# Performance work log

Hardware: AMD Instinct MI355X
Metric: run time of the kernel (lower is better)

The kernel has to match this reference:

```python
import jax, jax.numpy as jnp
import numpy as np

T, B, D, H = 512, 64, 1024, 1024

def setup_inputs() -> dict:
    key = jax.random.key(0)
    k1, k2, k3, k4, k5 = jax.random.split(key, 5)
    scale_x = np.sqrt(6.0) / np.sqrt(D + 4 * H)
    scale_h = np.sqrt(6.0) / np.sqrt(H + 4 * H)
    x_data = jax.random.normal(k1, (T, B, D), dtype=jnp.float32)
    # binary mask (1 = valid token), as used for variable-length sequences
    x_mask = (jax.random.uniform(k2, (T, B)) < 0.9).astype(jnp.float32)
    Wx = jax.random.uniform(k3, (4 * H, D), minval=-scale_x, maxval=scale_x, dtype=jnp.float32)
    bx = jax.random.uniform(k4, (4 * H,), minval=-scale_x, maxval=scale_x, dtype=jnp.float32)
    Wh = jax.random.uniform(k5, (4 * H, H), minval=-scale_h, maxval=scale_h, dtype=jnp.float32)
    return {"x_data": x_data, "x_mask": x_mask, "Wx": Wx, "bx": bx, "Wh": Wh}

def _lstm_forward(x_data, x_mask, Wx, bx, Wh):
    # Precompute input projections for all timesteps in one GEMM: [T,B,4H]
    xg = jnp.einsum('tbd,gd->tbg', x_data, Wx) + bx
    Hh = Wh.shape[1]

    def step(carry, inp):
        htm, ctm = carry
        xg_t, m_t = inp  # [B,4H], [B]
        gates = xg_t + htm @ Wh.T
        ig, fg, og, ct = jnp.split(gates, 4, axis=1)
        ig = jax.nn.sigmoid(ig)
        fg = jax.nn.sigmoid(fg)
        og = jax.nn.sigmoid(og)
        ct = jnp.tanh(ct)
        ct = fg * ctm + ig * ct
        ht = og * jnp.tanh(ct)
        m = m_t[:, None]
        ct = ct * m + ctm * (1.0 - m)
        ht = ht * m + htm * (1.0 - m)
        return (ht, ct), ht

    h0 = jnp.zeros((x_data.shape[1], Hh), dtype=x_data.dtype)
    c0 = jnp.zeros((x_data.shape[1], Hh), dtype=x_data.dtype)
    _, output = jax.lax.scan(step, (h0, c0), (xg, x_mask))
    return output  # [T,B,H]

def reference(x_data, x_mask, Wx, bx, Wh):
    return _lstm_forward(x_data, x_mask, Wx, bx, Wh)
```

## Files before the change

kernel.cpp:

```cpp
#include <hip/hip_runtime.h>
#include <hip/hip_bf16.h>

using f32x4  = __attribute__((ext_vector_type(4))) float;
using bf16x8 = __attribute__((ext_vector_type(8))) __bf16;
using u64    = unsigned long long;

#define T_DIM 512
#define B_DIM 64
#define D_DIM 1024
#define H_DIM 1024
#define G_DIM 4096
#define NWG   128
#define WGT   512

__global__ void f32_to_bf16_kernel(const float* __restrict__ src,
                                   __bf16* __restrict__ dst, long n) {
    long i = ((long)blockIdx.x * blockDim.x + threadIdx.x) * 8;
    if (i + 8 <= n) {
        f32x4 a = *(const f32x4*)(src + i);
        f32x4 b = *(const f32x4*)(src + i + 4);
        bf16x8 o;
        o[0] = (__bf16)a[0]; o[1] = (__bf16)a[1];
        o[2] = (__bf16)a[2]; o[3] = (__bf16)a[3];
        o[4] = (__bf16)b[0]; o[5] = (__bf16)b[1];
        o[6] = (__bf16)b[2]; o[7] = (__bf16)b[3];
        *(bf16x8*)(dst + i) = o;
    }
}

#define BM 128
#define BN 128
#define BK 64

__global__ __launch_bounds__(256) void gemm_xg_kernel(
    const __bf16* __restrict__ A,
    const __bf16* __restrict__ W,
    const float* __restrict__ bias,
    float* __restrict__ C,
    int M)
{
    (void)M;
    __shared__ __bf16 sA[BM * BK];
    __shared__ __bf16 sB[BN * BK];

    const int tid = threadIdx.x;
    const int wv  = tid >> 6;
    const int l   = tid & 63;
    const int wy  = wv >> 1, wx = wv & 1;
    const int bm  = blockIdx.y * BM;
    const int bn  = blockIdx.x * BN;
    const int n   = l & 15;
    const int q   = l >> 4;

    const int srow  = l >> 3;
    const int skoff = (l & 7) * 8;

    f32x4 acc[4][4];
    #pragma unroll
    for (int mt = 0; mt < 4; ++mt)
        #pragma unroll
        for (int nt = 0; nt < 4; ++nt)
            acc[mt][nt] = (f32x4){0.f, 0.f, 0.f, 0.f};

    for (int kt = 0; kt < D_DIM / BK; ++kt) {
        const int k0 = kt * BK;
        #pragma unroll
        for (int j = 0; j < 4; ++j) {
            const int rbase = (j * 4 + wv) * 8;
            const __bf16* ga = A + (long)(bm + rbase + srow) * D_DIM + k0 + skoff;
            const __bf16* gb = W + (long)(bn + rbase + srow) * D_DIM + k0 + skoff;
            __builtin_amdgcn_global_load_lds(
                (const __attribute__((address_space(1))) void*)ga,
                (__attribute__((address_space(3))) void*)(sA + rbase * BK), 16, 0, 0);
            __builtin_amdgcn_global_load_lds(
                (const __attribute__((address_space(1))) void*)gb,
                (__attribute__((address_space(3))) void*)(sB + rbase * BK), 16, 0, 0);
        }
        __syncthreads();

        #pragma unroll
        for (int ks = 0; ks < 2; ++ks) {
            bf16x8 af[4], bfr[4];
            #pragma unroll
            for (int mt = 0; mt < 4; ++mt) {
                int row = wy * 64 + mt * 16 + n;
                af[mt] = *(const bf16x8*)(sA + row * BK + ks * 32 + q * 8);
            }
            #pragma unroll
            for (int nt = 0; nt < 4; ++nt) {
                int col = wx * 64 + nt * 16 + n;
                bfr[nt] = *(const bf16x8*)(sB + col * BK + ks * 32 + q * 8);
            }
            #pragma unroll
            for (int mt = 0; mt < 4; ++mt)
                #pragma unroll
                for (int nt = 0; nt < 4; ++nt)
                    acc[mt][nt] = __builtin_amdgcn_mfma_f32_16x16x32_bf16(
                        af[mt], bfr[nt], acc[mt][nt], 0, 0, 0);
        }
        __syncthreads();
    }

    #pragma unroll
    for (int nt = 0; nt < 4; ++nt) {
        int col = bn + wx * 64 + nt * 16 + n;
        float b = bias[col];
        #pragma unroll
        for (int mt = 0; mt < 4; ++mt) {
            #pragma unroll
            for (int r = 0; r < 4; ++r) {
                int row = bm + wy * 64 + mt * 16 + q * 4 + r;
                C[(long)row * G_DIM + col] = acc[mt][nt][r] + b;
            }
        }
    }
}

__device__ __forceinline__ float fast_tanh(float x) {
    return 1.0f - 2.0f / (__expf(2.0f * x) + 1.0f);
}

__device__ __forceinline__ void grid_barrier(unsigned* __restrict__ flags,
                                             unsigned target, int tid, int wgid) {
    __syncthreads();
    if (tid == 0)
        __hip_atomic_store(&flags[wgid * 16], target, __ATOMIC_RELAXED,
                           __HIP_MEMORY_SCOPE_AGENT);
    if (tid < 64) {
        for (;;) {
            unsigned v0 = __hip_atomic_load(&flags[tid * 16],
                                            __ATOMIC_RELAXED, __HIP_MEMORY_SCOPE_AGENT);
            unsigned v1 = __hip_atomic_load(&flags[(tid + 64) * 16],
                                            __ATOMIC_RELAXED, __HIP_MEMORY_SCOPE_AGENT);
            if (__all((v0 >= target) & (v1 >= target))) break;
            __builtin_amdgcn_s_sleep(1);
        }
    }
    __syncthreads();
    __atomic_signal_fence(__ATOMIC_ACQUIRE);
}

__global__ __launch_bounds__(WGT)
__attribute__((amdgpu_waves_per_eu(2, 2)))
void lstm_scan_kernel(
    const __bf16* __restrict__ Whb,
    const float* __restrict__ xg,
    const float* __restrict__ mask,
    float* __restrict__ cst,
    __bf16* __restrict__ hbuf,
    float* __restrict__ out,
    unsigned* __restrict__ flags,
    int t0, int tc)
{
    __shared__ __align__(16) char shh[32768];
    __shared__ float sg[16][132];
    __shared__ unsigned short hp[16][32];

    const int tid  = threadIdx.x;
    const int wgid = blockIdx.x;
    const int rblk = wgid >> 5;
    const int ublk = wgid & 31;
    const int wv   = tid >> 6;
    const int l    = tid & 63;
    const int n    = l & 15;
    const int q    = l >> 4;
    const int gw   = wv >> 1;
    const int ch   = wv & 1;

    const int colg = gw * H_DIM + ublk * 32 + ch * 16 + n;

    bf16x8 breg[32];
    #pragma unroll
    for (int kk = 0; kk < 32; ++kk)
        breg[kk] = *(const bf16x8*)(Whb + (long)colg * H_DIM + kk * 32 + q * 8);

    const int grow_l = tid >> 5;
    const int u      = tid & 31;
    const int grow   = rblk * 16 + grow_l;
    const int ucol   = ublk * 32 + u;

    float c_r, h_r;
    if (t0 == 0) { c_r = 0.0f; h_r = 0.0f; }
    else {
        c_r = cst[grow * H_DIM + ucol];
        h_r = out[((long)(t0 - 1) * B_DIM + grow) * H_DIM + ucol];
    }

    float xc0, xc1, xc2, xc3, mkc;
    {
        const float* xr = xg + (long)grow * G_DIM + ucol;
        xc0 = xr[0]; xc1 = xr[H_DIM]; xc2 = xr[2 * H_DIM]; xc3 = xr[3 * H_DIM];
        mkc = mask[t0 * B_DIM + grow];
    }

    const int srow_lo = (l >> 3);
    const int sv      = l & 7;
    const int sq      = (l >> 1) & 3;
    const int sb      = (l & 1) * 8;

    for (int t = 0; t < tc; ++t) {
        const int gt = t0 + t;
        const __bf16* hread = hbuf + (long)(gt & 1) * (B_DIM * H_DIM);
        __bf16* hwrite = hbuf + (long)((gt + 1) & 1) * (B_DIM * H_DIM);
        const u64* h64 = (const u64*)hread;

        u64 hold[8];
        #pragma unroll
        for (int j = 0; j < 4; ++j) {
            const int kk = wv * 4 + j;
            hold[j * 2]     = __hip_atomic_load(
                h64 + (long)(rblk * 16 + srow_lo) * 256 + kk * 8 + sv,
                __ATOMIC_RELAXED, __HIP_MEMORY_SCOPE_AGENT);
            hold[j * 2 + 1] = __hip_atomic_load(
                h64 + (long)(rblk * 16 + 8 + srow_lo) * 256 + kk * 8 + sv,
                __ATOMIC_RELAXED, __HIP_MEMORY_SCOPE_AGENT);
        }
        #pragma unroll
        for (int j = 0; j < 4; ++j) {
            const int kk = wv * 4 + j;
            *(u64*)(shh + kk * 1024 + sq * 256 + srow_lo * 16 + sb)       = hold[j * 2];
            *(u64*)(shh + kk * 1024 + sq * 256 + (8 + srow_lo) * 16 + sb) = hold[j * 2 + 1];
        }
        __syncthreads();

        f32x4 ac0 = {0.f,0.f,0.f,0.f}, ac1 = {0.f,0.f,0.f,0.f};
        #pragma unroll
        for (int kk = 0; kk < 32; kk += 2) {
            bf16x8 f0 = *(const bf16x8*)(shh + (kk + 0) * 1024 + q * 256 + n * 16);
            bf16x8 f1 = *(const bf16x8*)(shh + (kk + 1) * 1024 + q * 256 + n * 16);
            ac0 = __builtin_amdgcn_mfma_f32_16x16x32_bf16(f0, breg[kk + 0], ac0, 0, 0, 0);
            ac1 = __builtin_amdgcn_mfma_f32_16x16x32_bf16(f1, breg[kk + 1], ac1, 0, 0, 0);
        }
        f32x4 acc = ac0 + ac1;

        {
            const int cw = gw * 32 + ch * 16 + n;
            #pragma unroll
            for (int r = 0; r < 4; ++r)
                sg[q * 4 + r][cw] = acc[r];
        }
        __syncthreads();

        float ig = xc0 + sg[grow_l][u];
        float fg = xc1 + sg[grow_l][32 + u];
        float og = xc2 + sg[grow_l][64 + u];
        float gg = xc3 + sg[grow_l][96 + u];

        float i_s = 1.0f / (1.0f + __expf(-ig));
        float f_s = 1.0f / (1.0f + __expf(-fg));
        float o_s = 1.0f / (1.0f + __expf(-og));
        float g_t = fast_tanh(gg);
        float c_new = f_s * c_r + i_s * g_t;
        float h_new = o_s * fast_tanh(c_new);
        float c_f = mkc * c_new + (1.0f - mkc) * c_r;
        float h_f = mkc * h_new + (1.0f - mkc) * h_r;
        c_r = c_f;
        h_r = h_f;

        hp[grow_l][u] = __builtin_bit_cast(unsigned short, (__bf16)h_f);
        __syncthreads();
        if (tid < 128) {
            const int prow = tid >> 3, pseg = tid & 7;
            u64 pk = *(const u64*)(&hp[prow][pseg * 4]);
            u64* dp = (u64*)((unsigned short*)hwrite +
                             (long)(rblk * 16 + prow) * H_DIM + ublk * 32 + pseg * 4);
            __hip_atomic_store(dp, pk, __ATOMIC_RELAXED, __HIP_MEMORY_SCOPE_AGENT);
        }

        out[((long)gt * B_DIM + grow) * H_DIM + ucol] = h_f;
        if (t == tc - 1) cst[grow * H_DIM + ucol] = c_f;

        if (t + 1 < tc) {
            const float* xr = xg + ((long)(t + 1) * B_DIM + grow) * G_DIM + ucol;
            xc0 = xr[0]; xc1 = xr[H_DIM]; xc2 = xr[2 * H_DIM]; xc3 = xr[3 * H_DIM];
            mkc = mask[(gt + 1) * B_DIM + grow];
        }

        grid_barrier(flags, (unsigned)(gt + 1), tid, wgid);
    }
}

extern "C" void kernel_launch(void* const* d_in, const int* in_sizes, int n_in,
                              void* d_out, int out_size, void* d_ws, size_t ws_size,
                              hipStream_t stream)
{
    (void)in_sizes; (void)n_in; (void)out_size;
    const float* x     = (const float*)d_in[0];
    const float* xmask = (const float*)d_in[1];
    const float* Wx    = (const float*)d_in[2];
    const float* bx    = (const float*)d_in[3];
    const float* Wh    = (const float*)d_in[4];
    float* out = (float*)d_out;

    char* ws = (char*)d_ws;
    __bf16*   Whb   = (__bf16*)(ws);
    __bf16*   Wxb   = (__bf16*)(ws + 8388608);
    __bf16*   hb    = (__bf16*)(ws + 16777216);
    float*    cst   = (float*)(ws + 16777216 + 262144);
    unsigned* flags = (unsigned*)(ws + 16777216 + 524288);
    char* dyn = ws + 16777216 + 1048576;

    long avail = (long)ws_size - (16777216L + 1048576L);
    const long per_t = (long)B_DIM * D_DIM * 2 + (long)B_DIM * G_DIM * 4;
    long Tc = avail > 0 ? avail / per_t : 2;
    if (Tc > T_DIM) Tc = T_DIM;
    Tc &= ~1L;
    if (Tc < 2) Tc = 2;

    __bf16* xb = (__bf16*)dyn;
    float*  xg = (float*)(dyn + Tc * (long)B_DIM * D_DIM * 2);

    hipMemsetAsync(ws + 16777216, 0, 1048576, stream);

    {
        long nw = (long)G_DIM * D_DIM;
        int nb = (int)(nw / 8 / 256);
        f32_to_bf16_kernel<<<nb, 256, 0, stream>>>(Wx, Wxb, nw);
        f32_to_bf16_kernel<<<nb, 256, 0, stream>>>(Wh, Whb, nw);
    }

    for (int t0 = 0; t0 < T_DIM; t0 += (int)Tc) {
        int tc = (int)((T_DIM - t0 < Tc) ? (long)(T_DIM - t0) : Tc);

        long nx = (long)tc * B_DIM * D_DIM;
        f32_to_bf16_kernel<<<(int)(nx / 8 / 256), 256, 0, stream>>>(
            x + (long)t0 * B_DIM * D_DIM, xb, nx);

        dim3 gg(G_DIM / BN, (tc * B_DIM) / BM);
        gemm_xg_kernel<<<gg, 256, 0, stream>>>(xb, Wxb, bx, xg, tc * B_DIM);

        const __bf16* Whb_a = Whb;
        const float*  xg_a  = xg;
        const float*  mask_a = xmask;
        float*  cst_a = cst;
        __bf16* hb_a  = hb;
        float*  out_a = out;
        unsigned* fl_a = flags;
        int t0_a = t0, tc_a = tc;
        void* args[] = {(void*)&Whb_a, (void*)&xg_a, (void*)&mask_a,
                        (void*)&cst_a, (void*)&hb_a, (void*)&out_a,
                        (void*)&fl_a, (void*)&t0_a, (void*)&tc_a};
        hipLaunchCooperativeKernel((void*)lstm_scan_kernel, dim3(NWG), dim3(WGT),
                                   args, 0, stream);
    }
}
```

Measured before the change: 2.532 ms.

## Remap gate columns per wave and narrow grid barrier to row-block peers

Each wave now computes all four gates for its own 4 hidden units, so the gate combine stays in a per-wave shared buffer. This removes two workgroup-wide __syncthreads per step, and h is packed with lane shuffles instead of a shared staging buffer. The grid barrier now waits only on the 32 workgroups that share the same batch row block, since only they produce the h rows this block reads. In exchange the out stores become vectorized but come from a quarter of the lanes, and correctness depends on the row-block independence of the recurrence.

```diff
diff --git a/kernel.cpp b/kernel.cpp
--- a/kernel.cpp
+++ b/kernel.cpp
@@ -121,18 +121,18 @@
 }
 
 __device__ __forceinline__ void grid_barrier(unsigned* __restrict__ flags,
-                                             unsigned target, int tid, int wgid) {
+                                             unsigned target, int tid,
+                                             int wgid, int rblk) {
     __syncthreads();
     if (tid == 0)
         __hip_atomic_store(&flags[wgid * 16], target, __ATOMIC_RELAXED,
                            __HIP_MEMORY_SCOPE_AGENT);
     if (tid < 64) {
+        const unsigned* fp = &flags[(rblk * 32 + (tid & 31)) * 16];
         for (;;) {
-            unsigned v0 = __hip_atomic_load(&flags[tid * 16],
-                                            __ATOMIC_RELAXED, __HIP_MEMORY_SCOPE_AGENT);
-            unsigned v1 = __hip_atomic_load(&flags[(tid + 64) * 16],
-                                            __ATOMIC_RELAXED, __HIP_MEMORY_SCOPE_AGENT);
-            if (__all((v0 >= target) & (v1 >= target))) break;
+            unsigned v = __hip_atomic_load(fp, __ATOMIC_RELAXED,
+                                           __HIP_MEMORY_SCOPE_AGENT);
+            if (__all(v >= target)) break;
             __builtin_amdgcn_s_sleep(1);
         }
     }
@@ -153,8 +153,7 @@
     int t0, int tc)
 {
     __shared__ __align__(16) char shh[32768];
-    __shared__ float sg[16][132];
-    __shared__ unsigned short hp[16][32];
+    __shared__ float sg[8][16 * 17];
 
     const int tid  = threadIdx.x;
     const int wgid = blockIdx.x;
@@ -164,20 +163,18 @@
     const int l    = tid & 63;
     const int n    = l & 15;
     const int q    = l >> 4;
-    const int gw   = wv >> 1;
-    const int ch   = wv & 1;
-
-    const int colg = gw * H_DIM + ublk * 32 + ch * 16 + n;
+
+    const int colg = ((n >> 2) << 10) + ublk * 32 + wv * 4 + (n & 3);
 
     bf16x8 breg[32];
     #pragma unroll
     for (int kk = 0; kk < 32; ++kk)
         breg[kk] = *(const bf16x8*)(Whb + (long)colg * H_DIM + kk * 32 + q * 8);
 
-    const int grow_l = tid >> 5;
-    const int u      = tid & 31;
-    const int grow   = rblk * 16 + grow_l;
-    const int ucol   = ublk * 32 + u;
+    const int rloc = l >> 2;
+    const int ui   = l & 3;
+    const int grow = rblk * 16 + rloc;
+    const int ucol = ublk * 32 + wv * 4 + ui;
 
     float c_r, h_r;
     if (t0 == 0) { c_r = 0.0f; h_r = 0.0f; }
@@ -199,6 +196,10 @@
     const int sb      = (l & 1) * 8;
 
     for (int t = 0; t < tc; ++t) {
+        #pragma unroll
+        for (int kk = 0; kk < 32; ++kk)
+            asm volatile("" : "+v"(breg[kk]));
+
         const int gt = t0 + t;
         const __bf16* hread = hbuf + (long)(gt & 1) * (B_DIM * H_DIM);
         __bf16* hwrite = hbuf + (long)((gt + 1) & 1) * (B_DIM * H_DIM);
@@ -233,18 +234,14 @@
         }
         f32x4 acc = ac0 + ac1;
 
-        {
-            const int cw = gw * 32 + ch * 16 + n;
-            #pragma unroll
-            for (int r = 0; r < 4; ++r)
-                sg[q * 4 + r][cw] = acc[r];
-        }
-        __syncthreads();
-
-        float ig = xc0 + sg[grow_l][u];
-        float fg = xc1 + sg[grow_l][32 + u];
-        float og = xc2 + sg[grow_l][64 + u];
-        float gg = xc3 + sg[grow_l][96 + u];
+        #pragma unroll
+        for (int r = 0; r < 4; ++r)
+            sg[wv][(q * 4 + r) * 17 + n] = acc[r];
+
+        float ig = xc0 + sg[wv][rloc * 17 + 0  + ui];
+        float fg = xc1 + sg[wv][rloc * 17 + 4  + ui];
+        float og = xc2 + sg[wv][rloc * 17 + 8  + ui];
+        float gg = xc3 + sg[wv][rloc * 17 + 12 + ui];
 
         float i_s = 1.0f / (1.0f + __expf(-ig));
         float f_s = 1.0f / (1.0f + __expf(-fg));
@@ -257,17 +254,24 @@
         c_r = c_f;
         h_r = h_f;
 
-        hp[grow_l][u] = __builtin_bit_cast(unsigned short, (__bf16)h_f);
-        __syncthreads();
-        if (tid < 128) {
-            const int prow = tid >> 3, pseg = tid & 7;
-            u64 pk = *(const u64*)(&hp[prow][pseg * 4]);
+        const int base = l & ~3;
+        float v0 = __shfl(h_f, base + 0);
+        float v1 = __shfl(h_f, base + 1);
+        float v2 = __shfl(h_f, base + 2);
+        float v3 = __shfl(h_f, base + 3);
+        if (ui == 0) {
+            f32x4 ov = {v0, v1, v2, v3};
+            *(f32x4*)(out + ((long)gt * B_DIM + grow) * H_DIM + ublk * 32 + wv * 4) = ov;
+            unsigned short b0 = __builtin_bit_cast(unsigned short, (__bf16)v0);
+            unsigned short b1 = __builtin_bit_cast(unsigned short, (__bf16)v1);
+            unsigned short b2 = __builtin_bit_cast(unsigned short, (__bf16)v2);
+            unsigned short b3 = __builtin_bit_cast(unsigned short, (__bf16)v3);
+            u64 pk = (u64)b0 | ((u64)b1 << 16) | ((u64)b2 << 32) | ((u64)b3 << 48);
             u64* dp = (u64*)((unsigned short*)hwrite +
-                             (long)(rblk * 16 + prow) * H_DIM + ublk * 32 + pseg * 4);
+                             (long)grow * H_DIM + ublk * 32 + wv * 4);
             __hip_atomic_store(dp, pk, __ATOMIC_RELAXED, __HIP_MEMORY_SCOPE_AGENT);
         }
 
-        out[((long)gt * B_DIM + grow) * H_DIM + ucol] = h_f;
         if (t == tc - 1) cst[grow * H_DIM + ucol] = c_f;
 
         if (t + 1 < tc) {
@@ -276,7 +280,7 @@
             mkc = mask[(gt + 1) * B_DIM + grow];
         }
 
-        grid_barrier(flags, (unsigned)(gt + 1), tid, wgid);
+        grid_barrier(flags, (unsigned)(gt + 1), tid, wgid, rblk);
     }
 }
 
```

Result: no change. 2.560 ms (+1.1%).
